# Kernel optimization log

Measured on AMD Instinct MI355X. Metric: run time of the kernel, lower is better.

## Reference

```python
import jax, jax.numpy as jnp
import numpy as np

V, D, S, B = 32000, 1024, 2048, 4
H = 4 * D


def _sinusoidal_pe(max_len, d):
    position = np.arange(max_len, dtype=np.float32)[:, None]
    div_term = np.exp(np.arange(0, d, 2, dtype=np.float32) * (-np.log(10000.0) / d))
    pe = np.zeros((max_len, d), dtype=np.float32)
    pe[:, 0::2] = np.sin(position * div_term)
    pe[:, 1::2] = np.cos(position * div_term)
    return jnp.asarray(pe)


def setup_inputs() -> dict:
    key = jax.random.key(0)
    ks = jax.random.split(key, 13)
    std = 1.0 / np.sqrt(D)
    stdh = 1.0 / np.sqrt(H)
    w = lambda k, shp, s: (jax.random.normal(k, shp, jnp.float32) * s)
    inp = {
        "tokens": jax.random.randint(ks[0], (B, S), 0, V),
        "emb": jax.random.normal(ks[1], (V, D), jnp.float32),
        "pe": _sinusoidal_pe(S, D),
        "l1_wk": w(ks[2], (D, D), std),
        "l1_wv": w(ks[3], (D, D), std),
        "l1_wo": w(ks[4], (D, D), std),
        "l1_w1": w(ks[5], (D, H), std),
        "l1_w2": w(ks[6], (H, D), stdh),
        "l2_wk": w(ks[7], (D, D), std),
        "l2_wv": w(ks[8], (D, D), std),
        "l2_wo": w(ks[9], (D, D), std),
        "l2_w1": w(ks[10], (D, H), std),
        "l2_w2": w(ks[11], (H, D), stdh),
        "w_out": w(ks[12], (D, V), std),
    }
    return inp


def _block(h, mask, wk, wv, wo, w1, w2):
    d = h.shape[-1]
    xq = h                      # W_q is identity
    xk = h @ wk                 # [B,S,D]
    xv = h @ wv
    scores = jnp.einsum("bsd,btd->bst", xq, xk) / np.sqrt(float(d)) + mask
    attn = jax.nn.softmax(scores, axis=-1)          # [B,S,S]
    h_attn = jnp.einsum("bst,btd->bsd", attn, xv) @ wo
    h_res = h + h_attn
    h_ffn = jnp.maximum(h_res @ w1, 0.0) @ w2
    return h_res + h_ffn


def reference(tokens, emb, pe, l1_wk, l1_wv, l1_wo, l1_w1, l1_w2,
              l2_wk, l2_wv, l2_wo, l2_w1, l2_w2, w_out):
    seq_len = tokens.shape[1]
    h = emb[tokens] + pe[None, :seq_len, :]
    # causal additive mask: -inf above diagonal
    mask = jnp.triu(jnp.full((seq_len, seq_len), -jnp.inf, jnp.float32), k=1)
    h = _block(h, mask, l1_wk, l1_wv, l1_wo, l1_w1, l1_w2)
    h = _block(h, mask, l2_wk, l2_wv, l2_wo, l2_w1, l2_w2)
    logits = h[:, -1, :] @ w_out  # [B, V]
    return logits
```

## Files before the change

kernel.cpp:

```cpp
#include <hip/hip_runtime.h>

#define S_LEN 2048
#define D_DIM 1024
#define H_DIM 4096
#define V_DIM 32000
#define B_SZ  4

typedef float  f32x4  __attribute__((ext_vector_type(4)));
typedef __bf16 bf16x8 __attribute__((ext_vector_type(8)));

__device__ __forceinline__ ushort f2bf(float f) {
    union { float f; unsigned u; } v; v.f = f;
    unsigned r = v.u + 0x7fffu + ((v.u >> 16) & 1u);
    return (ushort)(r >> 16);
}

__global__ void bt_wtranspose(const float* __restrict__ in, ushort* __restrict__ out,
                              int R, int C) {
    __shared__ ushort s[64][65];
    int r0 = blockIdx.y * 64, c0 = blockIdx.x * 64;
    int t = threadIdx.x;
    int lr = t >> 2, lc4 = (t & 3) * 16;
    const float* src = in + (size_t)(r0 + lr) * C + c0 + lc4;
#pragma unroll
    for (int j = 0; j < 4; ++j) {
        float4 v = ((const float4*)src)[j];
        s[lr][lc4 + 4 * j + 0] = f2bf(v.x);
        s[lr][lc4 + 4 * j + 1] = f2bf(v.y);
        s[lr][lc4 + 4 * j + 2] = f2bf(v.z);
        s[lr][lc4 + 4 * j + 3] = f2bf(v.w);
    }
    __syncthreads();
    int oc = t >> 2, orr = (t & 3) * 16;
    ushort tmp[16] __attribute__((aligned(16)));
#pragma unroll
    for (int j = 0; j < 16; ++j) tmp[j] = s[orr + j][oc];
    ushort* dst = out + (size_t)(c0 + oc) * R + r0 + orr;
    *(uint4*)dst        = *(uint4*)tmp;
    *(uint4*)(dst + 8)  = *(uint4*)(tmp + 8);
}

__global__ void bt_embed(const int* __restrict__ tokens, const float* __restrict__ emb,
                         const float* __restrict__ pe, float* __restrict__ h,
                         ushort* __restrict__ hbf) {
    int row = blockIdx.x;
    int s   = row & (S_LEN - 1);
    int tok = tokens[row];
    int t   = threadIdx.x;
    float4 v = ((const float4*)(emb + (size_t)tok * D_DIM))[t];
    float4 p = ((const float4*)(pe + (size_t)s * D_DIM))[t];
    v.x += p.x; v.y += p.y; v.z += p.z; v.w += p.w;
    ((float4*)(h + (size_t)row * D_DIM))[t] = v;
    uint2 pk;
    pk.x = (unsigned)f2bf(v.x) | ((unsigned)f2bf(v.y) << 16);
    pk.y = (unsigned)f2bf(v.z) | ((unsigned)f2bf(v.w) << 16);
    ((uint2*)(hbf + (size_t)row * D_DIM))[t] = pk;
}

#define EPI_F32  0
#define EPI_BF16 1
#define EPI_RELU 2
#define EPI_RES  3

#define VMWAIT(N) asm volatile("s_waitcnt vmcnt(%0)" :: "n"(N) : "memory")
#define SBAR()    __builtin_amdgcn_s_barrier()
#define MEMPIN()  asm volatile("" ::: "memory")
#define AS1 __attribute__((address_space(1)))
#define AS3 __attribute__((address_space(3)))

template <int BM, int BN, int EPI, bool CSKIP, bool KLIM, int SWZ>
__global__ __launch_bounds__(256, 2)
void bt_gemm8(const ushort* __restrict__ A, const ushort* __restrict__ B,
              float* Cf, ushort* Cb, const float* __restrict__ Res,
              int lda, int ldb, int ldc, int K,
              size_t strideA, size_t strideB, size_t strideC) {
    constexpr int MR = BM / 32;
    constexpr int NR = BN / 32;
    constexpr int Ak = BM / 64;
    constexpr int Bk = BN / 64;
    constexpr int G  = Ak + Bk;
    constexpr int HS = (BM + BN) * 32;

    __shared__ ushort lds[4][HS];

    int bm, bn;
    if (SWZ == 1) {
        int gx = gridDim.x, gy = gridDim.y;
        int id = blockIdx.y * gx + blockIdx.x;
        int xcd = id & 7, slot = id >> 3;
        int bandH = gy >> 3;
        bm = xcd * bandH + (slot % bandH);
        bn = slot / bandH;
    } else if (SWZ == 2) {
        int gx = gridDim.x;
        int id = blockIdx.y * gx + blockIdx.x;
        int xcd = id & 7, slot = id >> 3;
        int bandW = gx >> 3;
        bn = xcd * bandW + (slot % bandW);
        bm = slot / bandW;
    } else { bm = blockIdx.y; bn = blockIdx.x; }

    if (CSKIP && bn * BN >= (bm + 1) * BM) return;

    const int tid  = threadIdx.x;
    const int lane = tid & 63;
    const int wid  = tid >> 6;
    const int wr   = wid >> 1, wc = wid & 1;
    const int r15  = lane & 15, r4 = lane >> 4;
    const int lr   = lane >> 2;
    const int lsl  = lane & 3;
    const int kswz = (r4 ^ ((r15 >> 1) & 3)) * 8;

    const ushort* Ab = A + strideA * blockIdx.z + (size_t)bm * BM * lda;
    const ushort* Bb = B + strideB * blockIdx.z + (size_t)bn * BN * ldb;

    int NT = K >> 6;
    if (KLIM) { int lim = (bm + 1) * (BM / 64); if (lim < NT) NT = lim; }

    f32x4 acc[MR][NR];
#pragma unroll
    for (int m = 0; m < MR; ++m)
#pragma unroll
        for (int n = 0; n < NR; ++n) acc[m][n] = (f32x4){0.f, 0.f, 0.f, 0.f};

#define STAGE(hs)                                                                 \
    {                                                                             \
        const int t_ = (hs) >> 1, b_ = (hs) & 3;                                  \
        const int c_ = ((hs) & 1) * 4 + (lsl ^ ((lr >> 1) & 3));                  \
        _Pragma("unroll")                                                         \
        for (int j = 0; j < Ak; ++j) {                                            \
            int row = (wid + j * 4) * 16 + lr;                                    \
            __builtin_amdgcn_global_load_lds(                                     \
                (const AS1 void*)(Ab + (size_t)t_ * 64 + (size_t)row * lda + c_ * 8), \
                (AS3 void*)(&lds[b_][0] + (wid + j * 4) * 512), 16, 0, 0);        \
        }                                                                         \
        _Pragma("unroll")                                                         \
        for (int j = 0; j < Bk; ++j) {                                            \
            int row = (wid + j * 4) * 16 + lr;                                    \
            __builtin_amdgcn_global_load_lds(                                     \
                (const AS1 void*)(Bb + (size_t)t_ * 64 + (size_t)row * ldb + c_ * 8), \
                (AS3 void*)(&lds[b_][BM * 32] + (wid + j * 4) * 512), 16, 0, 0);  \
        }                                                                         \
    }

#define PHASE_COMPUTE(hs)                                                         \
    {                                                                             \
        const int b_ = (hs) & 3;                                                  \
        bf16x8 aq[MR], bq[NR];                                                    \
        _Pragma("unroll")                                                         \
        for (int m = 0; m < MR; ++m) {                                            \
            int row = wr * (BM / 2) + m * 16 + r15;                               \
            aq[m] = *(const bf16x8*)(&lds[b_][row * 32 + kswz]);                  \
        }                                                                         \
        _Pragma("unroll")                                                         \
        for (int n = 0; n < NR; ++n) {                                            \
            int col = wc * (BN / 2) + n * 16 + r15;                               \
            bq[n] = *(const bf16x8*)(&lds[b_][BM * 32 + col * 32 + kswz]);        \
        }                                                                         \
        __builtin_amdgcn_s_setprio(1);                                            \
        _Pragma("unroll")                                                         \
        for (int m = 0; m < MR; ++m)                                              \
            _Pragma("unroll")                                                     \
            for (int n = 0; n < NR; ++n)                                          \
                acc[m][n] = __builtin_amdgcn_mfma_f32_16x16x32_bf16(aq[m], bq[n], acc[m][n], 0, 0, 0); \
        __builtin_amdgcn_s_setprio(0);                                            \
    }

    STAGE(0); STAGE(1); STAGE(2);

    const int NH2 = 2 * NT;
    for (int hs = 0; hs < NH2 - 3; ++hs) {
        VMWAIT(2 * G); SBAR(); MEMPIN();
        STAGE(hs + 3);
        PHASE_COMPUTE(hs);
    }
    VMWAIT(2 * G); SBAR(); MEMPIN();
    PHASE_COMPUTE(NH2 - 3);
    VMWAIT(G); SBAR(); MEMPIN();
    PHASE_COMPUTE(NH2 - 2);
    VMWAIT(0); SBAR(); MEMPIN();
    PHASE_COMPUTE(NH2 - 1);

    size_t cz = strideC * blockIdx.z;
    const int rowb = bm * BM + wr * (BM / 2) + r4 * 4;
    const int colb = bn * BN + wc * (BN / 2) + r15;
#pragma unroll
    for (int m = 0; m < MR; ++m) {
#pragma unroll
        for (int r = 0; r < 4; ++r) {
            int row = rowb + m * 16 + r;
            size_t base = cz + (size_t)row * ldc + colb;
#pragma unroll
            for (int n = 0; n < NR; ++n) {
                float v = acc[m][n][r];
                size_t idx = base + n * 16;
                if (EPI == EPI_F32)       Cf[idx] = v;
                else if (EPI == EPI_BF16) Cb[idx] = f2bf(v);
                else if (EPI == EPI_RELU) Cb[idx] = f2bf(fmaxf(v, 0.f));
                else { float o = v + Res[idx]; Cf[idx] = o; Cb[idx] = f2bf(o); }
            }
        }
    }
#undef STAGE
#undef PHASE_COMPUTE
}

__device__ __forceinline__ float wred_max(float v) {
#pragma unroll
    for (int off = 32; off; off >>= 1) v = fmaxf(v, __shfl_xor(v, off));
    return v;
}
__device__ __forceinline__ float wred_sum(float v) {
#pragma unroll
    for (int off = 32; off; off >>= 1) v += __shfl_xor(v, off);
    return v;
}

__global__ void bt_softmax(const float* __restrict__ scores, ushort* __restrict__ probs) {
    int row = blockIdx.x;
    int s   = row & (S_LEN - 1);
    const float* src = scores + (size_t)row * S_LEN;
    ushort*      dst = probs  + (size_t)row * S_LEN;
    int tid = threadIdx.x;
    int nvalid = s + 1;

    float vals[8];
    float mx = -1e30f;
#pragma unroll
    for (int j = 0; j < 8; ++j) {
        int t = tid + j * 256;
        float v = (t < nvalid) ? src[t] * 0.03125f : -1e30f;
        vals[j] = v;
        mx = fmaxf(mx, v);
    }
    __shared__ float red[4], red2[4];
    mx = wred_max(mx);
    if ((tid & 63) == 0) red[tid >> 6] = mx;
    __syncthreads();
    mx = fmaxf(fmaxf(red[0], red[1]), fmaxf(red[2], red[3]));

    float sum = 0.f, ps[8];
#pragma unroll
    for (int j = 0; j < 8; ++j) {
        float p = exp2f((vals[j] - mx) * 1.44269504f);
        ps[j] = p; sum += p;
    }
    sum = wred_sum(sum);
    if ((tid & 63) == 0) red2[tid >> 6] = sum;
    __syncthreads();
    sum = red2[0] + red2[1] + red2[2] + red2[3];
    float inv = 1.0f / sum;
#pragma unroll
    for (int j = 0; j < 8; ++j) {
        int t = tid + j * 256;
        dst[t] = (t < nvalid) ? f2bf(ps[j] * inv) : (ushort)0;
    }
}

__global__ void bt_logits(const float* __restrict__ h, const float* __restrict__ wout,
                          float* __restrict__ out) {
    __shared__ float hl[4][128];
    int tid = threadIdx.x;
    int d0 = blockIdx.y * 128;
    if (tid < 128) {
#pragma unroll
        for (int b = 0; b < 4; ++b)
            hl[b][tid] = h[((size_t)b * S_LEN + (S_LEN - 1)) * D_DIM + d0 + tid];
    }
    __syncthreads();
    int v = blockIdx.x * 256 + tid;
    float a0 = 0, a1 = 0, a2 = 0, a3 = 0;
    for (int j = 0; j < 128; ++j) {
        float w = wout[(size_t)(d0 + j) * V_DIM + v];
        a0 += hl[0][j] * w; a1 += hl[1][j] * w;
        a2 += hl[2][j] * w; a3 += hl[3][j] * w;
    }
    atomicAdd(out + v, a0);
    atomicAdd(out + V_DIM + v, a1);
    atomicAdd(out + 2 * V_DIM + v, a2);
    atomicAdd(out + 3 * V_DIM + v, a3);
}

extern "C" void kernel_launch(void* const* d_in, const int* in_sizes, int n_in,
                              void* d_out, int out_size, void* d_ws, size_t ws_size,
                              hipStream_t stream) {
    const int*   tokens = (const int*)d_in[0];
    const float* emb    = (const float*)d_in[1];
    const float* pe     = (const float*)d_in[2];
    const float* wgt[10];
    for (int i = 0; i < 10; ++i) wgt[i] = (const float*)d_in[3 + i];
    const float* wout = (const float*)d_in[13];

    char* w = (char*)d_ws;
    size_t o = 0;
    auto take = [&](size_t sz) { char* p = w + o; o += (sz + 255) & ~(size_t)255; return p; };

    const size_t DD = (size_t)D_DIM * D_DIM * 2;
    const size_t DH = (size_t)D_DIM * H_DIM * 2;
    size_t wsz[10] = {DD, DD, DD, DH, DH, DD, DD, DD, DH, DH};
    ushort* wT[10];
    for (int i = 0; i < 10; ++i) wT[i] = (ushort*)take(wsz[i]);

    const size_t NROW = (size_t)B_SZ * S_LEN;
    float*  h0     = (float*)take(NROW * D_DIM * 4);
    float*  h1     = (float*)take(NROW * D_DIM * 4);
    ushort* hbf    = (ushort*)take(NROW * D_DIM * 2);
    ushort* hresbf = (ushort*)take(NROW * D_DIM * 2);
    ushort* xkbf   = (ushort*)take(NROW * D_DIM * 2);
    ushort* xvt    = (ushort*)take((size_t)D_DIM * NROW * 2);
    ushort* hattn  = (ushort*)take(NROW * D_DIM * 2);
    char*   G      = take((size_t)B_SZ * S_LEN * S_LEN * 4 + (size_t)B_SZ * S_LEN * S_LEN * 2);
    float*  scores = (float*)G;
    ushort* probs  = (ushort*)(G + (size_t)B_SZ * S_LEN * S_LEN * 4);
    ushort* tbf    = (ushort*)G;

    int wR[10] = {1024, 1024, 1024, 1024, 4096, 1024, 1024, 1024, 1024, 4096};
    int wC[10] = {1024, 1024, 1024, 4096, 1024, 1024, 1024, 1024, 4096, 1024};
    for (int i = 0; i < 10; ++i)
        bt_wtranspose<<<dim3(wC[i] / 64, wR[i] / 64), 256, 0, stream>>>(wgt[i], wT[i], wR[i], wC[i]);

    bt_embed<<<NROW, 256, 0, stream>>>(tokens, emb, pe, h0, hbf);

    auto layer = [&](ushort* wk, ushort* wv2, ushort* wo, ushort* w1, ushort* w2) {
        bt_gemm8<128, 128, EPI_BF16, false, false, 1><<<dim3(8, 64, 1), 256, 0, stream>>>(
            hbf, wk, nullptr, xkbf, nullptr, D_DIM, D_DIM, D_DIM, D_DIM, 0, 0, 0);
        bt_gemm8<128, 128, EPI_BF16, false, false, 2><<<dim3(64, 8, 1), 256, 0, stream>>>(
            wv2, hbf, nullptr, xvt, nullptr, D_DIM, D_DIM, (int)NROW, D_DIM, 0, 0, 0);
        bt_gemm8<128, 128, EPI_F32, true, false, 0><<<dim3(16, 16, B_SZ), 256, 0, stream>>>(
            hbf, xkbf, scores, nullptr, nullptr, D_DIM, D_DIM, S_LEN, D_DIM,
            (size_t)S_LEN * D_DIM, (size_t)S_LEN * D_DIM, (size_t)S_LEN * S_LEN);
        bt_softmax<<<NROW, 256, 0, stream>>>(scores, probs);
        bt_gemm8<128, 128, EPI_BF16, false, true, 0><<<dim3(8, 16, B_SZ), 256, 0, stream>>>(
            probs, xvt, nullptr, hattn, nullptr, S_LEN, (int)NROW, D_DIM, S_LEN,
            (size_t)S_LEN * S_LEN, (size_t)S_LEN, (size_t)S_LEN * D_DIM);
        bt_gemm8<128, 128, EPI_RES, false, false, 1><<<dim3(8, 64, 1), 256, 0, stream>>>(
            hattn, wo, h1, hresbf, h0, D_DIM, D_DIM, D_DIM, D_DIM, 0, 0, 0);
        bt_gemm8<128, 128, EPI_RELU, false, false, 1><<<dim3(32, 64, 1), 256, 0, stream>>>(
            hresbf, w1, nullptr, tbf, nullptr, D_DIM, D_DIM, H_DIM, D_DIM, 0, 0, 0);
        bt_gemm8<128, 128, EPI_RES, false, false, 1><<<dim3(8, 64, 1), 256, 0, stream>>>(
            tbf, w2, h0, hbf, h1, H_DIM, H_DIM, D_DIM, H_DIM, 0, 0, 0);
    };
    layer(wT[0], wT[1], wT[2], wT[3], wT[4]);
    layer(wT[5], wT[6], wT[7], wT[8], wT[9]);

    hipMemsetAsync(d_out, 0, (size_t)B_SZ * V_DIM * sizeof(float), stream);
    bt_logits<<<dim3(V_DIM / 256, D_DIM / 128), 256, 0, stream>>>(h0, wout, (float*)d_out);
}
```

Before: 881.9 us.

## Enlarge GEMM tiles, prefetch LDS fragments across phases, compute V then transpose

The GEMM kernel is generalized to take the warp count and warp grid as template parameters. The projection and attention GEMMs move to 256x128 tiles, and the FFN up-projection moves to 256x256 tiles with 8 waves. The main loop is restructured to read the next half-step's A fragments from LDS while the current MFMA cluster runs, with one barrier per half-step. The V projection now runs as a normal GEMM followed by a separate bf16 transpose kernel instead of a swapped-operand GEMM. Larger tiles cut redundant global and LDS traffic but raise register pressure, lower occupancy, and leave fewer blocks to fill the GPU.

```diff
diff --git a/kernel.cpp b/kernel.cpp
--- a/kernel.cpp
+++ b/kernel.cpp
@@ -38,6 +38,29 @@
     ushort* dst = out + (size_t)(c0 + oc) * R + r0 + orr;
     *(uint4*)dst        = *(uint4*)tmp;
     *(uint4*)(dst + 8)  = *(uint4*)(tmp + 8);
+}
+
+__global__ void bt_transpose(const ushort* __restrict__ in, ushort* __restrict__ out,
+                             int R, int C) {
+    __shared__ ushort s[64][65];
+    int r0 = blockIdx.y * 64, c0 = blockIdx.x * 64;
+    int t = threadIdx.x;
+    int lr = t >> 2, lc = (t & 3) * 16;
+    const ushort* src = in + (size_t)(r0 + lr) * C + c0 + lc;
+    uint4 v0 = ((const uint4*)src)[0];
+    uint4 v1 = ((const uint4*)src)[1];
+    ushort tin[16] __attribute__((aligned(16)));
+    *(uint4*)tin = v0; *(uint4*)(tin + 8) = v1;
+#pragma unroll
+    for (int j = 0; j < 16; ++j) s[lr][lc + j] = tin[j];
+    __syncthreads();
+    int oc = t >> 2, orr = (t & 3) * 16;
+    ushort tmp[16] __attribute__((aligned(16)));
+#pragma unroll
+    for (int j = 0; j < 16; ++j) tmp[j] = s[orr + j][oc];
+    ushort* dst = out + (size_t)(c0 + oc) * R + r0 + orr;
+    *(uint4*)dst       = *(uint4*)tmp;
+    *(uint4*)(dst + 8) = *(uint4*)(tmp + 8);
 }
 
 __global__ void bt_embed(const int* __restrict__ tokens, const float* __restrict__ emb,
@@ -68,18 +91,19 @@
 #define AS1 __attribute__((address_space(1)))
 #define AS3 __attribute__((address_space(3)))
 
-template <int BM, int BN, int EPI, bool CSKIP, bool KLIM, int SWZ>
-__global__ __launch_bounds__(256, 2)
-void bt_gemm8(const ushort* __restrict__ A, const ushort* __restrict__ B,
-              float* Cf, ushort* Cb, const float* __restrict__ Res,
-              int lda, int ldb, int ldc, int K,
-              size_t strideA, size_t strideB, size_t strideC) {
-    constexpr int MR = BM / 32;
-    constexpr int NR = BN / 32;
-    constexpr int Ak = BM / 64;
-    constexpr int Bk = BN / 64;
-    constexpr int G  = Ak + Bk;
-    constexpr int HS = (BM + BN) * 32;
+template <int BM, int BN, int NW, int WCc, int EPI, bool CSKIP, bool KLIM, int SWZ>
+__global__ __launch_bounds__(NW * 64, (NW == 8 ? 2 : 1))
+void bt_gemm(const ushort* __restrict__ A, const ushort* __restrict__ B,
+             float* Cf, ushort* Cb, const float* __restrict__ Res,
+             int lda, int ldb, int ldc, int K,
+             size_t strideA, size_t strideB, size_t strideC) {
+    constexpr int WRr = NW / WCc;
+    constexpr int MR  = BM / (16 * WRr);
+    constexpr int NR  = BN / (16 * WCc);
+    constexpr int Ak  = BM / (16 * NW);
+    constexpr int Bk  = BN / (16 * NW);
+    constexpr int G   = Ak + Bk;
+    constexpr int HS  = (BM + BN) * 32;
 
     __shared__ ushort lds[4][HS];
 
@@ -105,7 +129,7 @@
     const int tid  = threadIdx.x;
     const int lane = tid & 63;
     const int wid  = tid >> 6;
-    const int wr   = wid >> 1, wc = wid & 1;
+    const int wr   = wid / WCc, wc = wid % WCc;
     const int r15  = lane & 15, r4 = lane >> 4;
     const int lr   = lane >> 2;
     const int lsl  = lane & 3;
@@ -116,12 +140,15 @@
 
     int NT = K >> 6;
     if (KLIM) { int lim = (bm + 1) * (BM / 64); if (lim < NT) NT = lim; }
+    const int NH2 = 2 * NT;
 
     f32x4 acc[MR][NR];
 #pragma unroll
     for (int m = 0; m < MR; ++m)
 #pragma unroll
         for (int n = 0; n < NR; ++n) acc[m][n] = (f32x4){0.f, 0.f, 0.f, 0.f};
+
+    bf16x8 aqA[MR], aqB[MR], bq[NR];
 
 #define STAGE(hs)                                                                 \
     {                                                                             \
@@ -129,61 +156,77 @@
         const int c_ = ((hs) & 1) * 4 + (lsl ^ ((lr >> 1) & 3));                  \
         _Pragma("unroll")                                                         \
         for (int j = 0; j < Ak; ++j) {                                            \
-            int row = (wid + j * 4) * 16 + lr;                                    \
+            int row = (wid + j * NW) * 16 + lr;                                   \
             __builtin_amdgcn_global_load_lds(                                     \
                 (const AS1 void*)(Ab + (size_t)t_ * 64 + (size_t)row * lda + c_ * 8), \
-                (AS3 void*)(&lds[b_][0] + (wid + j * 4) * 512), 16, 0, 0);        \
+                (AS3 void*)(&lds[b_][0] + (wid + j * NW) * 512), 16, 0, 0);       \
         }                                                                         \
         _Pragma("unroll")                                                         \
         for (int j = 0; j < Bk; ++j) {                                            \
-            int row = (wid + j * 4) * 16 + lr;                                    \
+            int row = (wid + j * NW) * 16 + lr;                                   \
             __builtin_amdgcn_global_load_lds(                                     \
                 (const AS1 void*)(Bb + (size_t)t_ * 64 + (size_t)row * ldb + c_ * 8), \
-                (AS3 void*)(&lds[b_][BM * 32] + (wid + j * 4) * 512), 16, 0, 0);  \
+                (AS3 void*)(&lds[b_][BM * 32] + (wid + j * NW) * 512), 16, 0, 0); \
         }                                                                         \
     }
 
-#define PHASE_COMPUTE(hs)                                                         \
+#define READ_A(hs, dst)                                                           \
     {                                                                             \
         const int b_ = (hs) & 3;                                                  \
-        bf16x8 aq[MR], bq[NR];                                                    \
         _Pragma("unroll")                                                         \
         for (int m = 0; m < MR; ++m) {                                            \
-            int row = wr * (BM / 2) + m * 16 + r15;                               \
-            aq[m] = *(const bf16x8*)(&lds[b_][row * 32 + kswz]);                  \
+            int row = wr * (16 * MR) + m * 16 + r15;                              \
+            dst[m] = *(const bf16x8*)(&lds[b_][row * 32 + kswz]);                 \
         }                                                                         \
+    }
+
+#define READ_B(hs)                                                                \
+    {                                                                             \
+        const int b_ = (hs) & 3;                                                  \
         _Pragma("unroll")                                                         \
         for (int n = 0; n < NR; ++n) {                                            \
-            int col = wc * (BN / 2) + n * 16 + r15;                               \
+            int col = wc * (16 * NR) + n * 16 + r15;                              \
             bq[n] = *(const bf16x8*)(&lds[b_][BM * 32 + col * 32 + kswz]);        \
         }                                                                         \
-        __builtin_amdgcn_s_setprio(1);                                            \
-        _Pragma("unroll")                                                         \
-        for (int m = 0; m < MR; ++m)                                              \
-            _Pragma("unroll")                                                     \
-            for (int n = 0; n < NR; ++n)                                          \
-                acc[m][n] = __builtin_amdgcn_mfma_f32_16x16x32_bf16(aq[m], bq[n], acc[m][n], 0, 0, 0); \
-        __builtin_amdgcn_s_setprio(0);                                            \
-    }
-
-    STAGE(0); STAGE(1); STAGE(2);
-
-    const int NH2 = 2 * NT;
-    for (int hs = 0; hs < NH2 - 3; ++hs) {
-        VMWAIT(2 * G); SBAR(); MEMPIN();
+    }
+
+#define CLUSTER(aset)                                                             \
+    __builtin_amdgcn_s_setprio(1);                                                \
+    _Pragma("unroll")                                                             \
+    for (int m = 0; m < MR; ++m)                                                  \
+        _Pragma("unroll")                                                         \
+        for (int n = 0; n < NR; ++n)                                              \
+            acc[m][n] = __builtin_amdgcn_mfma_f32_16x16x32_bf16(aset[m], bq[n], acc[m][n], 0, 0, 0); \
+    __builtin_amdgcn_s_setprio(0);
+
+    STAGE(0); STAGE(1);
+    VMWAIT(G); SBAR(); MEMPIN();
+    STAGE(2);
+    READ_A(0, aqA);
+
+    for (int t = 0; t < NT - 1; ++t) {
+        const int hs = 2 * t;
+        VMWAIT(G); SBAR(); MEMPIN();
         STAGE(hs + 3);
-        PHASE_COMPUTE(hs);
-    }
-    VMWAIT(2 * G); SBAR(); MEMPIN();
-    PHASE_COMPUTE(NH2 - 3);
-    VMWAIT(G); SBAR(); MEMPIN();
-    PHASE_COMPUTE(NH2 - 2);
+        READ_B(hs);
+        READ_A(hs + 1, aqB);
+        CLUSTER(aqA);
+        VMWAIT(G); SBAR(); MEMPIN();
+        if (t < NT - 2) STAGE(hs + 4);
+        READ_B(hs + 1);
+        READ_A(hs + 2, aqA);
+        CLUSTER(aqB);
+    }
     VMWAIT(0); SBAR(); MEMPIN();
-    PHASE_COMPUTE(NH2 - 1);
+    READ_B(NH2 - 2);
+    READ_A(NH2 - 1, aqB);
+    CLUSTER(aqA);
+    READ_B(NH2 - 1);
+    CLUSTER(aqB);
 
     size_t cz = strideC * blockIdx.z;
-    const int rowb = bm * BM + wr * (BM / 2) + r4 * 4;
-    const int colb = bn * BN + wc * (BN / 2) + r15;
+    const int rowb = bm * BM + wr * (16 * MR) + r4 * 4;
+    const int colb = bn * BN + wc * (16 * NR) + r15;
 #pragma unroll
     for (int m = 0; m < MR; ++m) {
 #pragma unroll
@@ -202,7 +245,9 @@
         }
     }
 #undef STAGE
-#undef PHASE_COMPUTE
+#undef READ_A
+#undef READ_B
+#undef CLUSTER
 }
 
 __device__ __forceinline__ float wred_max(float v) {
@@ -322,22 +367,24 @@
     bt_embed<<<NROW, 256, 0, stream>>>(tokens, emb, pe, h0, hbf);
 
     auto layer = [&](ushort* wk, ushort* wv2, ushort* wo, ushort* w1, ushort* w2) {
-        bt_gemm8<128, 128, EPI_BF16, false, false, 1><<<dim3(8, 64, 1), 256, 0, stream>>>(
+        bt_gemm<256, 128, 4, 2, EPI_BF16, false, false, 1><<<dim3(8, 32), 256, 0, stream>>>(
             hbf, wk, nullptr, xkbf, nullptr, D_DIM, D_DIM, D_DIM, D_DIM, 0, 0, 0);
-        bt_gemm8<128, 128, EPI_BF16, false, false, 2><<<dim3(64, 8, 1), 256, 0, stream>>>(
-            wv2, hbf, nullptr, xvt, nullptr, D_DIM, D_DIM, (int)NROW, D_DIM, 0, 0, 0);
-        bt_gemm8<128, 128, EPI_F32, true, false, 0><<<dim3(16, 16, B_SZ), 256, 0, stream>>>(
+        bt_gemm<256, 128, 4, 2, EPI_BF16, false, false, 1><<<dim3(8, 32), 256, 0, stream>>>(
+            hbf, wv2, nullptr, hresbf, nullptr, D_DIM, D_DIM, D_DIM, D_DIM, 0, 0, 0);
+        bt_transpose<<<dim3(D_DIM / 64, NROW / 64), 256, 0, stream>>>(
+            hresbf, xvt, (int)NROW, D_DIM);
+        bt_gemm<256, 128, 4, 2, EPI_F32, true, false, 0><<<dim3(16, 8, B_SZ), 256, 0, stream>>>(
             hbf, xkbf, scores, nullptr, nullptr, D_DIM, D_DIM, S_LEN, D_DIM,
             (size_t)S_LEN * D_DIM, (size_t)S_LEN * D_DIM, (size_t)S_LEN * S_LEN);
         bt_softmax<<<NROW, 256, 0, stream>>>(scores, probs);
-        bt_gemm8<128, 128, EPI_BF16, false, true, 0><<<dim3(8, 16, B_SZ), 256, 0, stream>>>(
+        bt_gemm<256, 128, 4, 2, EPI_BF16, false, true, 0><<<dim3(8, 8, B_SZ), 256, 0, stream>>>(
             probs, xvt, nullptr, hattn, nullptr, S_LEN, (int)NROW, D_DIM, S_LEN,
             (size_t)S_LEN * S_LEN, (size_t)S_LEN, (size_t)S_LEN * D_DIM);
-        bt_gemm8<128, 128, EPI_RES, false, false, 1><<<dim3(8, 64, 1), 256, 0, stream>>>(
+        bt_gemm<256, 128, 4, 2, EPI_RES, false, false, 1><<<dim3(8, 32), 256, 0, stream>>>(
             hattn, wo, h1, hresbf, h0, D_DIM, D_DIM, D_DIM, D_DIM, 0, 0, 0);
-        bt_gemm8<128, 128, EPI_RELU, false, false, 1><<<dim3(32, 64, 1), 256, 0, stream>>>(
+        bt_gemm<256, 256, 8, 4, EPI_RELU, false, false, 1><<<dim3(16, 32), 512, 0, stream>>>(
             hresbf, w1, nullptr, tbf, nullptr, D_DIM, D_DIM, H_DIM, D_DIM, 0, 0, 0);
-        bt_gemm8<128, 128, EPI_RES, false, false, 1><<<dim3(8, 64, 1), 256, 0, stream>>>(
+        bt_gemm<256, 128, 4, 2, EPI_RES, false, false, 1><<<dim3(8, 32), 256, 0, stream>>>(
             tbf, w2, h0, hbf, h1, H_DIM, H_DIM, D_DIM, H_DIM, 0, 0, 0);
     };
     layer(wT[0], wT[1], wT[2], wT[3], wT[4]);
```

Result: slower. 988.5 us (+12.1%).
